# Optimization experiments

Hardware: AMD Instinct MI355X
Metric: run time of the kernel (lower is better)

Reference implementation:

```python
import jax, jax.numpy as jnp
import numpy as np
import math

B, L, HID = 2, 2048, 1024
H, DK, RATIO, SHARED, TOPK = 4, 64, 4, 1, 2
EXP_V = 2
DV = DK * EXP_V
KEY_DIM = H * DK
VAL_DIM = KEY_DIM * EXP_V
HE = H * RATIO
KS = 4
EPS = 1e-5


def _silu(x):
    return x * jax.nn.sigmoid(x)


def _dwconv_causal(x, w):
    # x: (B, L, C), w: (C, KS); causal depthwise short conv
    xp = jnp.pad(x, ((0, 0), (KS - 1, 0), (0, 0))).transpose(0, 2, 1)
    y = jax.lax.conv_general_dilated(xp, w[:, None, :], (1,), 'VALID',
                                     feature_group_count=w.shape[0],
                                     dimension_numbers=('NCH', 'OIH', 'NCH'))
    return y.transpose(0, 2, 1)


def _l2norm(x):
    return x * jax.lax.rsqrt(jnp.sum(x * x, -1, keepdims=True) + 1e-6)


def _forward(hidden_states, Wq, Wk, Wv, Wb, Wa, Wg, Wo, conv_q, conv_k, conv_v,
             Wq_exp, Wk_exp, W_gate, A_log, dt_bias, norm_w):
    x = hidden_states
    q = _silu(_dwconv_causal(x @ Wq.T, conv_q)).reshape(B, L, H, DK)
    k = _silu(_dwconv_causal(x @ Wk.T, conv_k)).reshape(B, L, H, DK)
    v = _silu(_dwconv_causal(x @ Wv.T, conv_v)).reshape(B, L, H, DV)
    # per-head expert expansion -> (B,L,H,RATIO,DK)
    qe = jnp.einsum('blhd,hkd->blhk', q, Wq_exp).reshape(B, L, H, RATIO, DK)
    ke = jnp.einsum('blhd,hkd->blhk', k, Wk_exp).reshape(B, L, H, RATIO, DK)
    qe = _l2norm(qe) * (DK ** -0.5)
    ke = _l2norm(ke)
    # token-policy top-k routing over non-shared experts
    logits = jnp.einsum('blhd,nd->blhn', q, W_gate)
    scores = jax.nn.softmax(logits.astype(jnp.float32), axis=-1)
    tw, ti = jax.lax.top_k(scores, TOPK)
    tw = tw / jnp.sum(tw, -1, keepdims=True)
    full = jnp.sum(jax.nn.one_hot(ti + SHARED, RATIO, dtype=tw.dtype) * tw[..., None], axis=-2)
    full = full.at[..., :SHARED].set(1.0 / SHARED)
    w_r = (full / jnp.sum(full, -1, keepdims=True)).astype(x.dtype)  # (B,L,H,RATIO)
    mask = (w_r > 0).astype(x.dtype)
    beta = jax.nn.sigmoid(x @ Wb.T).reshape(B, L, H, RATIO) * mask
    g = -jnp.exp(A_log).reshape(H, RATIO) * jax.nn.softplus((x @ Wa.T) + dt_bias).reshape(B, L, H, RATIO)
    g = g * mask  # unrouted memories: exp(0)=1, no decay, no update
    # gated delta-rule recurrence over HE = H*RATIO memories
    qs = qe.reshape(B, L, HE, DK).transpose(1, 0, 2, 3)
    ks_ = ke.reshape(B, L, HE, DK).transpose(1, 0, 2, 3)
    vs = jnp.broadcast_to(v[:, :, :, None, :], (B, L, H, RATIO, DV)).reshape(B, L, HE, DV).transpose(1, 0, 2, 3)
    bs = beta.reshape(B, L, HE).transpose(1, 0, 2)
    gs = g.reshape(B, L, HE).transpose(1, 0, 2)

    def step(S, xs):
        qt, kt, vt, bt, gt = xs
        S = S * jnp.exp(gt)[..., None, None]
        kv = jnp.einsum('bhk,bhkv->bhv', kt, S)
        S = S + jnp.einsum('bhk,bhv->bhkv', kt, (vt - kv) * bt[..., None])
        return S, jnp.einsum('bhk,bhkv->bhv', qt, S)

    S0 = jnp.zeros((B, HE, DK, DV), x.dtype)
    _, o = jax.lax.scan(step, S0, (qs, ks_, vs, bs, gs))
    o = o.transpose(1, 0, 2, 3).reshape(B, L, H, RATIO, DV)
    o = jnp.einsum('blhe,blhev->blhv', w_r, o)
    # FusedRMSNormSwishGate + output projection
    gate = (x @ Wg.T).reshape(B, L, H, DV)
    o = o * jax.lax.rsqrt(jnp.mean(o * o, -1, keepdims=True) + EPS) * norm_w * _silu(gate)
    return o.reshape(B, L, VAL_DIM) @ Wo.T


def setup_inputs():
    keys = jax.random.split(jax.random.key(0), 18)
    n = lambda i, shp, sc=1.0: jax.random.normal(keys[i], shp, jnp.float32) * sc
    A = jax.random.uniform(keys[14], (HE,), jnp.float32, 1e-3, 16.0)
    dt = jnp.exp(jax.random.uniform(keys[15], (HE,), jnp.float32) * (math.log(0.1) - math.log(0.001)) + math.log(0.001))
    dt = jnp.clip(dt, 1e-4, None)
    return {
        'hidden_states': n(0, (B, L, HID)),
        'Wq': n(1, (KEY_DIM, HID), HID ** -0.5),
        'Wk': n(2, (KEY_DIM, HID), HID ** -0.5),
        'Wv': n(3, (VAL_DIM, HID), HID ** -0.5),
        'Wb': n(4, (HE, HID), HID ** -0.5),
        'Wa': n(5, (HE, HID), HID ** -0.5),
        'Wg': n(6, (VAL_DIM, HID), HID ** -0.5),
        'Wo': n(7, (HID, VAL_DIM), VAL_DIM ** -0.5),
        'conv_q': n(8, (KEY_DIM, KS), 0.5),
        'conv_k': n(9, (KEY_DIM, KS), 0.5),
        'conv_v': n(10, (VAL_DIM, KS), 0.5),
        'Wq_exp': n(11, (H, RATIO * DK, DK), DK ** -0.5),
        'Wk_exp': n(12, (H, RATIO * DK, DK), DK ** -0.5),
        'W_gate': n(13, (RATIO - SHARED, DK), DK ** -0.5),
        'A_log': jnp.log(A),
        'dt_bias': dt + jnp.log(-jnp.expm1(-dt)),
        'norm_w': jnp.ones((DV,), jnp.float32),
    }


def reference(hidden_states, Wq, Wk, Wv, Wb, Wa, Wg, Wo, conv_q, conv_k, conv_v,
              Wq_exp, Wk_exp, W_gate, A_log, dt_bias, norm_w):
    return _forward(hidden_states, Wq, Wk, Wv, Wb, Wa, Wg, Wo, conv_q, conv_k, conv_v,
                    Wq_exp, Wk_exp, W_gate, A_log, dt_bias, norm_w)
```

## Files before the change

kernel.cpp:

```cpp
#include <hip/hip_runtime.h>
#include <hip/hip_bf16.h>
#include <math.h>

#define B_    2
#define L_    2048
#define HID_  1024
#define H_    4
#define DK_   64
#define RATIO_ 4
#define HE_   16
#define DV_   128
#define T_    64
#define NC_   32
#define SPITCH 72
#define APITCH 68
#define NCAT  1408

typedef __attribute__((ext_vector_type(8))) short short8;
typedef __attribute__((ext_vector_type(4))) float f32x4;

__device__ __forceinline__ float sigmoidf_(float x){ return 1.f/(1.f+expf(-x)); }
__device__ __forceinline__ ushort f2bf(float x){
  __hip_bfloat16 h = __float2bfloat16(x);
  return *reinterpret_cast<ushort*>(&h);
}
__device__ __forceinline__ float bf2f(ushort u){
  union { uint32_t i; float f; } v; v.i = ((uint32_t)u) << 16; return v.f;
}
__device__ __forceinline__ uint32_t pk2(float a, float b){
  return ((uint32_t)f2bf(b) << 16) | f2bf(a);
}
__device__ __forceinline__ void unpk8(uint4 w, float* f){
  f[0]=bf2f((ushort)(w.x&0xffff)); f[1]=bf2f((ushort)(w.x>>16));
  f[2]=bf2f((ushort)(w.y&0xffff)); f[3]=bf2f((ushort)(w.y>>16));
  f[4]=bf2f((ushort)(w.z&0xffff)); f[5]=bf2f((ushort)(w.z>>16));
  f[6]=bf2f((ushort)(w.w&0xffff)); f[7]=bf2f((ushort)(w.w>>16));
}

__global__ __launch_bounds__(256) void cast_bf16(const float* __restrict__ in,
                                                 ushort* __restrict__ out, int n)
{
  int i = blockIdx.x*256 + threadIdx.x;
  if (i < n) out[i] = f2bf(in[i]);
}

__global__ __launch_bounds__(256) void concat_wcat(const float* __restrict__ Wk,
    const float* __restrict__ Wv, const float* __restrict__ Wg,
    const float* __restrict__ Wb, const float* __restrict__ Wa,
    ushort* __restrict__ Wcat)
{
  int idx = blockIdx.x*256 + threadIdx.x;
  if (idx >= NCAT*1024) return;
  int r = idx >> 10, cc = idx & 1023;
  float v = 0.f;
  if      (r < 256)  v = Wk[(size_t)r*1024 + cc];
  else if (r < 768)  v = Wv[(size_t)(r-256)*1024 + cc];
  else if (r < 1280) v = Wg[(size_t)(r-768)*1024 + cc];
  else if (r < 1296) v = Wb[(size_t)(r-1280)*1024 + cc];
  else if (r < 1312) v = Wa[(size_t)(r-1296)*1024 + cc];
  Wcat[idx] = f2bf(v);
}

__global__ __launch_bounds__(256) void gemm_bf16(
    const ushort* __restrict__ A, int lda,
    const ushort* __restrict__ Bm, int ldb,
    float* __restrict__ C, int ldc, int K)
{
  __shared__ ushort As[128*32];
  __shared__ ushort Bs[128*32];
  const int tid  = threadIdx.x;
  const int wave = tid >> 6, lane = tid & 63;
  const int row0 = blockIdx.y*128, col0 = blockIdx.x*128;
  const int wr = (wave >> 1) * 64, wc = (wave & 1) * 64;
  const int frow = lane & 15;
  const int fko  = (lane >> 4) << 3;
  f32x4 acc[4][4];
  #pragma unroll
  for (int i=0;i<4;i++)
    #pragma unroll
    for (int j=0;j<4;j++) acc[i][j] = (f32x4){0.f,0.f,0.f,0.f};
  for (int k0 = 0; k0 < K; k0 += 32) {
    #pragma unroll
    for (int cc = 0; cc < 2; cc++) {
      int c  = wave*128 + cc*64 + lane;
      int r  = c >> 2;
      int ko = (c & 3) << 3;
      __builtin_amdgcn_global_load_lds(
        (const __attribute__((address_space(1))) void*)(A + (size_t)(row0+r)*lda + k0 + ko),
        (__attribute__((address_space(3))) void*)(As + (size_t)(wave*128 + cc*64)*8),
        16, 0, 0);
      __builtin_amdgcn_global_load_lds(
        (const __attribute__((address_space(1))) void*)(Bm + (size_t)(col0+r)*ldb + k0 + ko),
        (__attribute__((address_space(3))) void*)(Bs + (size_t)(wave*128 + cc*64)*8),
        16, 0, 0);
    }
    __syncthreads();
    short8 af[4], bfv[4];
    #pragma unroll
    for (int mi=0;mi<4;mi++)
      af[mi] = *reinterpret_cast<const short8*>(&As[(wr + mi*16 + frow)*32 + fko]);
    #pragma unroll
    for (int ni=0;ni<4;ni++)
      bfv[ni] = *reinterpret_cast<const short8*>(&Bs[(wc + ni*16 + frow)*32 + fko]);
    #pragma unroll
    for (int mi=0;mi<4;mi++)
      #pragma unroll
      for (int ni=0;ni<4;ni++)
        acc[mi][ni] = __builtin_amdgcn_mfma_f32_16x16x32_bf16(af[mi], bfv[ni], acc[mi][ni], 0, 0, 0);
    __syncthreads();
  }
  const int ocol = lane & 15;
  const int orow = (lane >> 4) << 2;
  #pragma unroll
  for (int mi=0;mi<4;mi++)
    #pragma unroll
    for (int ni=0;ni<4;ni++) {
      size_t base = (size_t)(row0 + wr + mi*16 + orow)*ldc + (col0 + wc + ni*16 + ocol);
      #pragma unroll
      for (int q=0;q<4;q++) C[base + (size_t)q*ldc] = acc[mi][ni][q];
    }
}

__global__ __launch_bounds__(256) void gemm_expand_bf16(
    const ushort* __restrict__ qc_bf, const ushort* __restrict__ kc_bf,
    const ushort* __restrict__ Wqeb, const ushort* __restrict__ Wkeb,
    ushort* __restrict__ qeb, ushort* __restrict__ keb)
{
  const int z = blockIdx.z;
  const int hh = z & 3;
  const ushort* A  = (z < 4 ? qc_bf : kc_bf) + hh*64;
  const ushort* Bm = (z < 4 ? Wqeb  : Wkeb ) + (size_t)hh*16384;
  ushort* C        = (z < 4 ? qeb   : keb  ) + hh*256;
  const int lda = 256, ldb = 64, ldc = 1024, K = 64;
  __shared__ ushort As[128*32];
  __shared__ ushort Bs[128*32];
  const int tid  = threadIdx.x;
  const int wave = tid >> 6, lane = tid & 63;
  const int row0 = blockIdx.y*128, col0 = blockIdx.x*128;
  const int wr = (wave >> 1) * 64, wc = (wave & 1) * 64;
  const int frow = lane & 15;
  const int fko  = (lane >> 4) << 3;
  f32x4 acc[4][4];
  #pragma unroll
  for (int i=0;i<4;i++)
    #pragma unroll
    for (int j=0;j<4;j++) acc[i][j] = (f32x4){0.f,0.f,0.f,0.f};
  for (int k0 = 0; k0 < K; k0 += 32) {
    #pragma unroll
    for (int cc = 0; cc < 2; cc++) {
      int c  = wave*128 + cc*64 + lane;
      int r  = c >> 2;
      int ko = (c & 3) << 3;
      __builtin_amdgcn_global_load_lds(
        (const __attribute__((address_space(1))) void*)(A + (size_t)(row0+r)*lda + k0 + ko),
        (__attribute__((address_space(3))) void*)(As + (size_t)(wave*128 + cc*64)*8),
        16, 0, 0);
      __builtin_amdgcn_global_load_lds(
        (const __attribute__((address_space(1))) void*)(Bm + (size_t)(col0+r)*ldb + k0 + ko),
        (__attribute__((address_space(3))) void*)(Bs + (size_t)(wave*128 + cc*64)*8),
        16, 0, 0);
    }
    __syncthreads();
    short8 af[4], bfv[4];
    #pragma unroll
    for (int mi=0;mi<4;mi++)
      af[mi] = *reinterpret_cast<const short8*>(&As[(wr + mi*16 + frow)*32 + fko]);
    #pragma unroll
    for (int ni=0;ni<4;ni++)
      bfv[ni] = *reinterpret_cast<const short8*>(&Bs[(wc + ni*16 + frow)*32 + fko]);
    #pragma unroll
    for (int mi=0;mi<4;mi++)
      #pragma unroll
      for (int ni=0;ni<4;ni++)
        acc[mi][ni] = __builtin_amdgcn_mfma_f32_16x16x32_bf16(af[mi], bfv[ni], acc[mi][ni], 0, 0, 0);
    __syncthreads();
  }
  const int ocol = lane & 15;
  const int orow = (lane >> 4) << 2;
  #pragma unroll
  for (int mi=0;mi<4;mi++)
    #pragma unroll
    for (int ni=0;ni<4;ni++) {
      size_t base = (size_t)(row0 + wr + mi*16 + orow)*ldc + (col0 + wc + ni*16 + ocol);
      #pragma unroll
      for (int q=0;q<4;q++) C[base + (size_t)q*ldc] = f2bf(acc[mi][ni][q]);
    }
}

__global__ __launch_bounds__(256) void gemm_f32_db(const float* __restrict__ A, int lda,
    const float* __restrict__ Bm, int ldb, float* __restrict__ C, int ldc,
    int M, int N, int K)
{
  __shared__ float As[2][32][64];
  __shared__ float Bs[2][32][64];
  const int tid = threadIdx.x;
  const int row0 = blockIdx.y * 64;
  const int col0 = blockIdx.x * 64;
  const int tx = tid & 15, ty = tid >> 4;
  const int r0s = tid >> 3;
  const int k4s = (tid & 7) << 2;
  float4 av0, av1, bv0, bv1;

  av0 = *(const float4*)&A[(size_t)(row0 + r0s)*lda + k4s];
  av1 = *(const float4*)&A[(size_t)(row0 + r0s + 32)*lda + k4s];
  bv0 = (col0 + r0s < N) ? *(const float4*)&Bm[(size_t)(col0 + r0s)*ldb + k4s] : make_float4(0,0,0,0);
  bv1 = (col0 + r0s + 32 < N) ? *(const float4*)&Bm[(size_t)(col0 + r0s + 32)*ldb + k4s] : make_float4(0,0,0,0);
  As[0][k4s+0][r0s] = av0.x; As[0][k4s+1][r0s] = av0.y; As[0][k4s+2][r0s] = av0.z; As[0][k4s+3][r0s] = av0.w;
  As[0][k4s+0][r0s+32] = av1.x; As[0][k4s+1][r0s+32] = av1.y; As[0][k4s+2][r0s+32] = av1.z; As[0][k4s+3][r0s+32] = av1.w;
  Bs[0][k4s+0][r0s] = bv0.x; Bs[0][k4s+1][r0s] = bv0.y; Bs[0][k4s+2][r0s] = bv0.z; Bs[0][k4s+3][r0s] = bv0.w;
  Bs[0][k4s+0][r0s+32] = bv1.x; Bs[0][k4s+1][r0s+32] = bv1.y; Bs[0][k4s+2][r0s+32] = bv1.z; Bs[0][k4s+3][r0s+32] = bv1.w;
  __syncthreads();

  float acc[4][4] = {};
  const int nt = K >> 5;
  for (int kt = 0; kt < nt; ++kt) {
    const int p = kt & 1;
    if (kt + 1 < nt) {
      int k0 = (kt+1) << 5;
      av0 = *(const float4*)&A[(size_t)(row0 + r0s)*lda + k0 + k4s];
      av1 = *(const float4*)&A[(size_t)(row0 + r0s + 32)*lda + k0 + k4s];
      bv0 = (col0 + r0s < N) ? *(const float4*)&Bm[(size_t)(col0 + r0s)*ldb + k0 + k4s] : make_float4(0,0,0,0);
      bv1 = (col0 + r0s + 32 < N) ? *(const float4*)&Bm[(size_t)(col0 + r0s + 32)*ldb + k0 + k4s] : make_float4(0,0,0,0);
    }
    #pragma unroll
    for (int kk = 0; kk < 32; kk++) {
      float4 a4 = *(const float4*)&As[p][kk][ty*4];
      float4 b4 = *(const float4*)&Bs[p][kk][tx*4];
      float a[4] = {a4.x,a4.y,a4.z,a4.w};
      float b[4] = {b4.x,b4.y,b4.z,b4.w};
      #pragma unroll
      for (int i=0;i<4;i++)
        #pragma unroll
        for (int j=0;j<4;j++) acc[i][j] += a[i]*b[j];
    }
    if (kt + 1 < nt) {
      const int q = p ^ 1;
      As[q][k4s+0][r0s] = av0.x; As[q][k4s+1][r0s] = av0.y; As[q][k4s+2][r0s] = av0.z; As[q][k4s+3][r0s] = av0.w;
      As[q][k4s+0][r0s+32] = av1.x; As[q][k4s+1][r0s+32] = av1.y; As[q][k4s+2][r0s+32] = av1.z; As[q][k4s+3][r0s+32] = av1.w;
      Bs[q][k4s+0][r0s] = bv0.x; Bs[q][k4s+1][r0s] = bv0.y; Bs[q][k4s+2][r0s] = bv0.z; Bs[q][k4s+3][r0s] = bv0.w;
      Bs[q][k4s+0][r0s+32] = bv1.x; Bs[q][k4s+1][r0s+32] = bv1.y; Bs[q][k4s+2][r0s+32] = bv1.z; Bs[q][k4s+3][r0s+32] = bv1.w;
    }
    __syncthreads();
  }
  #pragma unroll
  for (int i=0;i<4;i++) {
    int r = row0 + ty*4 + i;
    #pragma unroll
    for (int j=0;j<4;j++) {
      int cc = col0 + tx*4 + j;
      if (cc < N) C[(size_t)r*ldc + cc] = acc[i][j];
    }
  }
}

__global__ __launch_bounds__(256) void conv_silu(const float* __restrict__ in, int ild,
    const float* __restrict__ w, float* __restrict__ outf, ushort* __restrict__ outb,
    int C, int total)
{
  int n = blockIdx.x*256 + threadIdx.x;
  if (n >= total) return;
  int c = n % C;
  int t = (n / C) % L_;
  int b = n / (C*L_);
  float acc = 0.f;
  #pragma unroll
  for (int s = 0; s < 4; s++) {
    int tt = t - 3 + s;
    if (tt >= 0) acc += in[((size_t)b*L_ + tt)*ild + c] * w[c*4+s];
  }
  float y = acc * sigmoidf_(acc);
  if (outf) outf[n] = y;
  if (outb) outb[n] = f2bf(y);
}

__global__ __launch_bounds__(256) void routing(const float* __restrict__ qc,
    const float* __restrict__ kvgba, const float* __restrict__ Wg3,
    const float* __restrict__ A_log, const float* __restrict__ dt_bias,
    float* __restrict__ w_buf, float* __restrict__ bt_T, float* __restrict__ g_T)
{
  int n = blockIdx.x*256 + threadIdx.x;
  int h  = n & 3;
  int bl = n >> 2;
  const float* q = qc + (size_t)bl*256 + h*64;
  float l0=0.f, l1=0.f, l2=0.f;
  for (int d=0; d<64; d++) {
    float qd = q[d];
    l0 += qd*Wg3[d]; l1 += qd*Wg3[64+d]; l2 += qd*Wg3[128+d];
  }
  float mx = fmaxf(l0, fmaxf(l1, l2));
  float e0 = expf(l0-mx), e1 = expf(l1-mx), e2 = expf(l2-mx);
  float inv_s = 1.f/(e0+e1+e2);
  float p0 = e0*inv_s, p1 = e1*inv_s, p2 = e2*inv_s;
  int m1 = 0; float pm1 = p0;
  if (p1 > pm1) { m1 = 1; pm1 = p1; }
  if (p2 > pm1) { m1 = 2; pm1 = p2; }
  int ia = (m1==0) ? 1 : 0;
  int ib = (m1==2) ? 1 : 2;
  float pa = (m1==0) ? p1 : p0;
  float pb = (m1==2) ? p1 : p2;
  int   m2  = (pb > pa) ? ib : ia;
  float pm2 = (pb > pa) ? pb : pa;
  float inv_w = 1.f/(pm1 + pm2);
  float w1 = 0.5f*pm1*inv_w;
  float w2 = 0.5f*pm2*inv_w;
  #pragma unroll
  for (int r = 0; r < 4; r++) {
    float wr = (r==0) ? 0.5f : (((r-1)==m1) ? w1 : (((r-1)==m2) ? w2 : 0.f));
    int he = h*4 + r;
    w_buf[(size_t)bl*16 + he] = wr;
    float mask = (wr > 0.f) ? 1.f : 0.f;
    bt_T[(size_t)he*4096 + bl] = mask * sigmoidf_(kvgba[(size_t)bl*NCAT + 1280 + he]);
    float av = kvgba[(size_t)bl*NCAT + 1296 + he] + dt_bias[he];
    float sp = fmaxf(av, 0.f) + log1pf(expf(-fabsf(av)));
    g_T[(size_t)he*4096 + bl] = -expf(A_log[he]) * sp * mask;
  }
}

__device__ __forceinline__ f32x4 tile64(const ushort* Am, int r0,
                                        const ushort* Bm, int c0, int lane)
{
  f32x4 acc = {0.f,0.f,0.f,0.f};
  const int fr = lane & 15, fo = (lane >> 4) << 3;
  #pragma unroll
  for (int kk = 0; kk < 2; ++kk) {
    short8 a = *reinterpret_cast<const short8*>(&Am[(r0+fr)*SPITCH + fo + kk*32]);
    short8 b = *reinterpret_cast<const short8*>(&Bm[(c0+fr)*SPITCH + fo + kk*32]);
    acc = __builtin_amdgcn_mfma_f32_16x16x32_bf16(a, b, acc, 0, 0, 0);
  }
  return acc;
}

__global__ __launch_bounds__(256,2) void scan_chunk_mfma(
    const ushort* __restrict__ keb, const ushort* __restrict__ qeb,
    const ushort* __restrict__ vcb, const float* __restrict__ bt_T,
    const float* __restrict__ g_T, ushort* __restrict__ o0b,
    ushort* __restrict__ Qtb, ushort* __restrict__ Mcb, ushort* __restrict__ Bcb)
{
  __shared__ float smem[18496];
  ushort* Kbf = (ushort*)smem;
  ushort* Qbf = (ushort*)(smem + 2304);
  ushort* KTD = (ushort*)(smem + 4608);
  float*  Af  = smem + 6912;
  ushort* Pf  = (ushort*)(smem + 6912);
  ushort* UV  = (ushort*)(smem + 11264);
  float*  cgs = smem + 18176;
  float*  bts = cgs + 64;
  float*  bGs = bts + 64;
  float*  Ds  = bGs + 64;
  float*  gams= Ds + 64;

  const int id = blockIdx.x;
  const int c  = id >> 5;
  const int s  = id & 31;
  const int h  = s & 3;
  const int b  = (s >> 2) & 1;
  const int r  = s >> 3;
  const int he = h*4 + r;
  const int bhe = b*HE_ + he;
  const int tid = threadIdx.x;
  const int wave = tid >> 6, lane = tid & 63;
  const size_t l0 = (size_t)b*L_ + (size_t)c*T_;

  const int tr = tid >> 2;
  const int sg = tid & 3;
  float kf[16], qf[16];
  uint4 vw0, vw1, vw2, vw3;
  float sk, sq;
  {
    const uint4* kp = (const uint4*)(keb + (l0+tr)*1024 + he*64 + sg*16);
    const uint4* qp = (const uint4*)(qeb + (l0+tr)*1024 + he*64 + sg*16);
    uint4 kv[2] = {kp[0], kp[1]};
    uint4 qv[2] = {qp[0], qp[1]};
    unpk8(kv[0], kf); unpk8(kv[1], kf+8);
    unpk8(qv[0], qf); unpk8(qv[1], qf+8);
    float ssk = 0.f, ssq = 0.f;
    #pragma unroll
    for (int i=0;i<16;i++){ ssk += kf[i]*kf[i]; ssq += qf[i]*qf[i]; }
    ssk += __shfl_xor(ssk, 1); ssk += __shfl_xor(ssk, 2);
    ssq += __shfl_xor(ssq, 1); ssq += __shfl_xor(ssq, 2);
    sk = rsqrtf(ssk + 1e-6f);
    sq = rsqrtf(ssq + 1e-6f) * 0.125f;
    const uint4* vp = (const uint4*)(vcb + (l0+tr)*512 + h*128 + sg*32);
    vw0 = vp[0]; vw1 = vp[1]; vw2 = vp[2]; vw3 = vp[3];
  }
  if (tid < 64) {
    float g  = g_T[(size_t)he*4096 + l0 + tid];
    float bt = bt_T[(size_t)he*4096 + l0 + tid];
    float cg = g;
    #pragma unroll
    for (int off = 1; off < 64; off <<= 1) {
      float o = __shfl_up(cg, off);
      if (tid >= off) cg += o;
    }
    float cg63 = __shfl(cg, 63);
    cgs[tid] = cg; bts[tid] = bt;
    float gm = expf(cg);
    gams[tid] = gm; bGs[tid] = bt*gm; Ds[tid] = expf(cg63 - cg);
  }
  __syncthreads();
  {
    float Dt = Ds[tr];
    uint2* kdst = (uint2*)(Kbf + tr*SPITCH + sg*16);
    uint2* qdst = (uint2*)(Qbf + tr*SPITCH + sg*16);
    #pragma unroll
    for (int i=0;i<4;i++){
      kdst[i] = make_uint2(pk2(kf[4*i+0]*sk, kf[4*i+1]*sk), pk2(kf[4*i+2]*sk, kf[4*i+3]*sk));
      qdst[i] = make_uint2(pk2(qf[4*i+0]*sq, qf[4*i+1]*sq), pk2(qf[4*i+2]*sq, qf[4*i+3]*sq));
    }
    float skD = sk*Dt;
    #pragma unroll
    for (int i=0;i<16;i++){
      int d = sg*16 + i;
      KTD[d*SPITCH + tr] = f2bf(kf[i]*skD);
    }
    uint4* vdst = (uint4*)(UV + tr*128 + sg*32);
    vdst[0] = vw0; vdst[1] = vw1; vdst[2] = vw2; vdst[3] = vw3;
  }
  __syncthreads();
  {
    const int r0 = wave*16;
    #pragma unroll
    for (int ct=0; ct<4; ++ct) {
      f32x4 acc = tile64(Kbf, r0, Kbf, ct*16, lane);
      int t = r0 + ((lane>>4)<<2);
      int ss = ct*16 + (lane&15);
      #pragma unroll
      for (int q=0;q<4;q++){
        int tq = t + q;
        Af[tq*APITCH + ss] = (ss < tq) ? bts[tq]*expf(cgs[tq]-cgs[ss])*acc[q] : 0.f;
      }
    }
  }
  __syncthreads();
  float u[64];
  if (tid < 192) {
    if (tid < 128) {
      const ushort* Vb = UV;
      #pragma unroll
      for (int ss=0;ss<64;++ss) u[ss] = bts[ss]*bf2f(Vb[ss*128 + tid]);
    } else {
      #pragma unroll
      for (int ss=0;ss<64;++ss) u[ss] = bGs[ss]*bf2f(Kbf[ss*SPITCH + (tid-128)]);
    }
  }
  __syncthreads();
  if (tid < 192) {
    #pragma unroll
    for (int t=1;t<64;++t) {
      const float4* Ar = (const float4*)(Af + t*APITCH);
      float p0=0.f,p1=0.f,p2=0.f,p3=0.f;
      #pragma unroll
      for (int s4=0; s4*4<t; ++s4) {
        float4 a = Ar[s4];
        p0 += a.x*u[s4*4+0]; p1 += a.y*u[s4*4+1];
        p2 += a.z*u[s4*4+2]; p3 += a.w*u[s4*4+3];
      }
      u[t] -= (p0+p1)+(p2+p3);
    }
    ushort* Ut = UV;
    uint4* dst = (uint4*)&Ut[tid*SPITCH];
    #pragma unroll
    for (int i=0;i<8;++i)
      dst[i] = make_uint4(pk2(u[8*i+0],u[8*i+1]), pk2(u[8*i+2],u[8*i+3]),
                          pk2(u[8*i+4],u[8*i+5]), pk2(u[8*i+6],u[8*i+7]));
  }
  __syncthreads();
  {
    const int r0 = wave*16;
    f32x4 accs[4];
    #pragma unroll
    for (int ct=0; ct<4; ++ct) accs[ct] = tile64(Qbf, r0, Kbf, ct*16, lane);
    __syncthreads();
    #pragma unroll
    for (int ct=0; ct<4; ++ct) {
      int t = r0 + ((lane>>4)<<2);
      int ss = ct*16 + (lane&15);
      #pragma unroll
      for (int q=0;q<4;q++){
        int tq = t + q;
        float val = (ss <= tq) ? expf(cgs[tq]-cgs[ss])*accs[ct][q] : 0.f;
        Pf[tq*SPITCH + ss] = f2bf(val);
      }
    }
  }
  __syncthreads();
  {
    const int r0 = wave*16;
    const float gend = expf(cgs[63]);
    const ushort* Ut = UV;
    const ushort* UtK = UV + 128*SPITCH;
    const size_t bb = ((size_t)bhe*NC_ + c)*(size_t)(64*128);
    const size_t pb = ((size_t)bhe*NC_ + c)*(size_t)(64*64);
    #pragma unroll
    for (int jt=0; jt<8; ++jt) {
      f32x4 acc = tile64(Pf, r0, Ut, jt*16, lane);
      int t = r0 + ((lane>>4)<<2);
      int j = jt*16 + (lane&15);
      #pragma unroll
      for (int q=0;q<4;q++)
        o0b[((l0 + t + q)*HE_ + he)*DV_ + j] = f2bf(acc[q]);
    }
    #pragma unroll
    for (int jt=0; jt<8; ++jt) {
      f32x4 acc = tile64(KTD, r0, Ut, jt*16, lane);
      int i = r0 + ((lane>>4)<<2);
      int j = jt*16 + (lane&15);
      #pragma unroll
      for (int q=0;q<4;q++)
        Bcb[bb + (size_t)(i+q)*128 + j] = f2bf(acc[q]);
    }
    #pragma unroll
    for (int ct=0; ct<4; ++ct) {
      f32x4 acc = tile64(KTD, r0, UtK, ct*16, lane);
      int i = r0 + ((lane>>4)<<2);
      int m = ct*16 + (lane&15);
      #pragma unroll
      for (int q=0;q<4;q++){
        float val = -acc[q];
        int row = i + q;
        if (row == m) val += gend;
        int pc = (((m>>3)^(row&7))<<3) | (m&7);
        Mcb[pb + (size_t)row*64 + pc] = f2bf(val);
      }
    }
    #pragma unroll
    for (int ct=0; ct<4; ++ct) {
      f32x4 acc = tile64(Pf, r0, UtK, ct*16, lane);
      int t = r0 + ((lane>>4)<<2);
      int m = ct*16 + (lane&15);
      #pragma unroll
      for (int q=0;q<4;q++){
        int row = t + q;
        int pc = (((m>>3)^(row&7))<<3) | (m&7);
        Qtb[pb + (size_t)row*64 + pc] = f2bf(gams[row]*bf2f(Qbf[row*SPITCH + m]) - acc[q]);
      }
    }
  }
}

__device__ __forceinline__ void stage_qm(const ushort* __restrict__ src, ushort* dst,
                                         int wave, int lane)
{
  #pragma unroll
  for (int pass = 0; pass < 2; ++pass){
    int idx = pass*256 + wave*64 + lane;
    __builtin_amdgcn_global_load_lds(
      (const __attribute__((address_space(1))) void*)(src + (size_t)idx*8),
      (__attribute__((address_space(3))) void*)(dst + (size_t)idx*8), 16, 0, 0);
  }
}

__global__ __launch_bounds__(256) void compose_correct(
    const ushort* __restrict__ Mcb, const ushort* __restrict__ Bcb,
    const ushort* __restrict__ Qtb, ushort* __restrict__ o_corrb)
{
  __shared__ ushort Ql[2][4096];
  __shared__ ushort Ml[2][4096];
  __shared__ float SSl[1024];
  const int s   = blockIdx.x;
  const int h   = s & 3;
  const int b   = (s >> 2) & 1;
  const int r   = s >> 3;
  const int he  = h*4 + r;
  const int bhe = b*HE_ + he;
  const int j0  = blockIdx.y * 16;
  const int tid = threadIdx.x;
  const int wave = tid >> 6, lane = tid & 63;
  const int rw = tid >> 2;
  const int jg = tid & 3;
  const int rsw = rw & 7;

  for (int id = tid; id < 1024; id += 256) SSl[id] = 0.f;

  stage_qm(Mcb + (size_t)(bhe*NC_)*4096, Ml[0], wave, lane);
  float4 bcur;
  {
    uint2 bw = *(const uint2*)&Bcb[(size_t)(bhe*NC_)*8192 + rw*128 + j0 + jg*4];
    bcur = make_float4(bf2f((ushort)(bw.x&0xffff)), bf2f((ushort)(bw.x>>16)),
                       bf2f((ushort)(bw.y&0xffff)), bf2f((ushort)(bw.y>>16)));
  }
  __syncthreads();

  int p = 0;
  for (int c = 0; c < NC_; ++c){
    float4 bnext = make_float4(0.f,0.f,0.f,0.f);
    if (c+1 < NC_){
      stage_qm(Qtb + (size_t)(bhe*NC_ + c + 1)*4096, Ql[p^1], wave, lane);
      if (c+1 < NC_-1){
        stage_qm(Mcb + (size_t)(bhe*NC_ + c + 1)*4096, Ml[p^1], wave, lane);
        uint2 bw = *(const uint2*)&Bcb[(size_t)(bhe*NC_ + c + 1)*8192 + rw*128 + j0 + jg*4];
        bnext = make_float4(bf2f((ushort)(bw.x&0xffff)), bf2f((ushort)(bw.x>>16)),
                            bf2f((ushort)(bw.y&0xffff)), bf2f((ushort)(bw.y>>16)));
      }
    }
    const float4* SS4 = (const float4*)SSl;
    float4 oa = make_float4(0.f,0.f,0.f,0.f);
    if (c > 0){
      const ushort* Qr = Ql[p] + rw*64;
      #pragma unroll
      for (int gb = 0; gb < 8; ++gb){
        uint4 w = *(const uint4*)&Qr[(gb ^ rsw) << 3];
        float f[8]; unpk8(w, f);
        #pragma unroll
        for (int e = 0; e < 8; ++e){
          float4 sv = SS4[(gb*8+e)*4 + jg];
          oa.x += f[e]*sv.x; oa.y += f[e]*sv.y; oa.z += f[e]*sv.z; oa.w += f[e]*sv.w;
        }
      }
    }
    {
      size_t oi = (((size_t)b*L_ + c*T_ + rw)*HE_ + he)*DV_ + j0 + jg*4;
      *(uint2*)&o_corrb[oi] = make_uint2(pk2(oa.x, oa.y), pk2(oa.z, oa.w));
    }
    float4 ns = bcur;
    if (c < NC_-1){
      const ushort* Mr = Ml[p] + rw*64;
      #pragma unroll
      for (int gb = 0; gb < 8; ++gb){
        uint4 w = *(const uint4*)&Mr[(gb ^ rsw) << 3];
        float f[8]; unpk8(w, f);
        #pragma unroll
        for (int e = 0; e < 8; ++e){
          float4 sv = SS4[(gb*8+e)*4 + jg];
          ns.x += f[e]*sv.x; ns.y += f[e]*sv.y; ns.z += f[e]*sv.z; ns.w += f[e]*sv.w;
        }
      }
    }
    __syncthreads();
    if (c < NC_-1) *(float4*)&SSl[rw*16 + jg*4] = ns;
    __syncthreads();
    p ^= 1;
    bcur = bnext;
  }
}

__global__ __launch_bounds__(128) void combine(const ushort* __restrict__ o0b,
    const ushort* __restrict__ o_corrb, const float* __restrict__ w_buf,
    const float* __restrict__ kvgba, const float* __restrict__ norm_w,
    ushort* __restrict__ o_fin)
{
  int n  = blockIdx.x;
  int h  = n & 3;
  int bl = n >> 2;
  int j  = threadIdx.x;
  size_t wb = (size_t)bl*16 + h*4;
  size_t ob = wb*128 + j;
  float oc = 0.f;
  #pragma unroll
  for (int r = 0; r < 4; r++){
    size_t oi = ob + (size_t)r*128;
    oc += w_buf[wb+r] * (bf2f(o0b[oi]) + bf2f(o_corrb[oi]));
  }
  float ss = oc*oc;
  #pragma unroll
  for (int off = 32; off > 0; off >>= 1) ss += __shfl_xor(ss, off);
  __shared__ float red[2];
  if ((threadIdx.x & 63) == 0) red[threadIdx.x >> 6] = ss;
  __syncthreads();
  float mean = (red[0] + red[1]) * (1.f/128.f);
  float sc = rsqrtf(mean + 1e-5f);
  float gv = kvgba[(size_t)bl*NCAT + 768 + h*128 + j];
  o_fin[(size_t)bl*512 + h*128 + j] = f2bf(oc * sc * norm_w[j] * (gv * sigmoidf_(gv)));
}

extern "C" void kernel_launch(void* const* d_in, const int* in_sizes, int n_in,
                              void* d_out, int out_size, void* d_ws, size_t ws_size,
                              hipStream_t stream)
{
  (void)in_sizes; (void)n_in; (void)out_size; (void)ws_size;
  const float* x       = (const float*)d_in[0];
  const float* Wq      = (const float*)d_in[1];
  const float* Wk      = (const float*)d_in[2];
  const float* Wv      = (const float*)d_in[3];
  const float* Wb      = (const float*)d_in[4];
  const float* Wa      = (const float*)d_in[5];
  const float* Wg      = (const float*)d_in[6];
  const float* Wo      = (const float*)d_in[7];
  const float* conv_q  = (const float*)d_in[8];
  const float* conv_k  = (const float*)d_in[9];
  const float* conv_v  = (const float*)d_in[10];
  const float* Wq_exp  = (const float*)d_in[11];
  const float* Wk_exp  = (const float*)d_in[12];
  const float* W_gate  = (const float*)d_in[13];
  const float* A_log   = (const float*)d_in[14];
  const float* dt_bias = (const float*)d_in[15];
  const float* norm_w  = (const float*)d_in[16];
  float* out = (float*)d_out;

  const size_t BL = (size_t)B_*L_;
  float* p = (float*)d_ws;
  float* q_lin  = p; p += BL*256;
  float* kvgba  = p; p += BL*NCAT;
  float* q_conv = p; p += BL*256;
  float* w_buf  = p; p += BL*16;
  float* bt_T   = p; p += BL*16;
  float* g_T    = p; p += BL*16;
  ushort* o0b   = (ushort*)p; p += BL*16*64;
  ushort* o_corrb=(ushort*)p; p += BL*16*64;
  ushort* Mcb   = (ushort*)p; p += (size_t)B_*HE_*NC_*2048;
  ushort* Qtb   = (ushort*)p; p += (size_t)B_*HE_*NC_*2048;
  ushort* Bcb   = (ushort*)p; p += (size_t)B_*HE_*NC_*4096;
  ushort* v_convb=(ushort*)p; p += BL*256;
  ushort* xb    = (ushort*)p; p += BL*512;
  ushort* Wcat  = (ushort*)p; p += (NCAT*1024)/2;
  ushort* qc_bf = (ushort*)p; p += BL*128;
  ushort* kc_bf = (ushort*)p; p += BL*128;
  ushort* qeb   = (ushort*)p; p += BL*512;
  ushort* keb   = (ushort*)p; p += BL*512;
  ushort* Wqeb  = (ushort*)p; p += 32768;
  ushort* Wkeb  = (ushort*)p; p += 32768;
  ushort* Wob   = (ushort*)p; p += 262144;
  ushort* o_finb= (ushort*)p; p += BL*256;

  concat_wcat<<<dim3((NCAT*1024+255)/256), dim3(256), 0, stream>>>(Wk, Wv, Wg, Wb, Wa, Wcat);
  { int n = (int)(BL*1024); cast_bf16<<<dim3((n+255)/256), dim3(256), 0, stream>>>(x, xb, n); }
  { int n = 65536;  cast_bf16<<<dim3((n+255)/256), dim3(256), 0, stream>>>(Wq_exp, Wqeb, n); }
  { int n = 65536;  cast_bf16<<<dim3((n+255)/256), dim3(256), 0, stream>>>(Wk_exp, Wkeb, n); }
  { int n = 524288; cast_bf16<<<dim3((n+255)/256), dim3(256), 0, stream>>>(Wo, Wob, n); }

  gemm_f32_db<<<dim3(4, 64), dim3(256), 0, stream>>>(x, 1024, Wq, 1024, q_lin, 256, 4096, 256, 1024);
  gemm_bf16<<<dim3(NCAT/128, 32), dim3(256), 0, stream>>>(xb, 1024, Wcat, 1024, kvgba, NCAT, 1024);

  { int tot = B_*L_*256; conv_silu<<<dim3((tot+255)/256), dim3(256), 0, stream>>>(q_lin, 256, conv_q, q_conv, qc_bf, 256, tot); }
  { int tot = B_*L_*256; conv_silu<<<dim3((tot+255)/256), dim3(256), 0, stream>>>(kvgba, NCAT, conv_k, (float*)nullptr, kc_bf, 256, tot); }
  { int tot = B_*L_*512; conv_silu<<<dim3((tot+255)/256), dim3(256), 0, stream>>>(kvgba + 256, NCAT, conv_v, (float*)nullptr, v_convb, 512, tot); }

  routing<<<dim3(64), dim3(256), 0, stream>>>(q_conv, kvgba, W_gate, A_log, dt_bias,
                                              w_buf, bt_T, g_T);

  gemm_expand_bf16<<<dim3(2, 32, 8), dim3(256), 0, stream>>>(qc_bf, kc_bf, Wqeb, Wkeb, qeb, keb);

  scan_chunk_mfma<<<dim3(NC_*HE_*B_), dim3(256), 0, stream>>>(keb, qeb, v_convb, bt_T, g_T,
                                                              o0b, Qtb, Mcb, Bcb);
  compose_correct<<<dim3(32, 8), dim3(256), 0, stream>>>(Mcb, Bcb, Qtb, o_corrb);
  combine<<<dim3(B_*L_*H_), dim3(128), 0, stream>>>(o0b, o_corrb, w_buf, kvgba, norm_w, o_finb);

  gemm_bf16<<<dim3(8, 32), dim3(256), 0, stream>>>(o_finb, 512, Wob, 512, out, 1024, 512);
}
```

Measured before the change: 358.1 us.

## Stage scan outputs in LDS for coalesced stores; split compose into single-wave blocks

In the chunk scan kernel, the o0 and Bc tiles are now written into shared memory first and then copied out to global memory as 16-byte vectorised stores, replacing scattered 2-byte stores. The compose_correct kernel is restructured from 256-thread blocks covering 16 value columns to 64-thread single-wave blocks covering 8 columns, which doubles the grid. Each thread now owns a full row and 8 columns. The aim is better store coalescing and more parallel blocks for the serial chunk recurrence, at the cost of extra syncs and reuse of shared memory in the scan kernel, and more redundant M/Q staging per block in compose.

```diff
diff --git a/kernel.cpp b/kernel.cpp
--- a/kernel.cpp
+++ b/kernel.cpp
@@ -486,33 +486,16 @@
   __syncthreads();
   {
     const int r0 = wave*16;
+    const int orow = (lane >> 4) << 2;
     const float gend = expf(cgs[63]);
     const ushort* Ut = UV;
     const ushort* UtK = UV + 128*SPITCH;
     const size_t bb = ((size_t)bhe*NC_ + c)*(size_t)(64*128);
     const size_t pb = ((size_t)bhe*NC_ + c)*(size_t)(64*64);
     #pragma unroll
-    for (int jt=0; jt<8; ++jt) {
-      f32x4 acc = tile64(Pf, r0, Ut, jt*16, lane);
-      int t = r0 + ((lane>>4)<<2);
-      int j = jt*16 + (lane&15);
-      #pragma unroll
-      for (int q=0;q<4;q++)
-        o0b[((l0 + t + q)*HE_ + he)*DV_ + j] = f2bf(acc[q]);
-    }
-    #pragma unroll
-    for (int jt=0; jt<8; ++jt) {
-      f32x4 acc = tile64(KTD, r0, Ut, jt*16, lane);
-      int i = r0 + ((lane>>4)<<2);
-      int j = jt*16 + (lane&15);
-      #pragma unroll
-      for (int q=0;q<4;q++)
-        Bcb[bb + (size_t)(i+q)*128 + j] = f2bf(acc[q]);
-    }
-    #pragma unroll
     for (int ct=0; ct<4; ++ct) {
       f32x4 acc = tile64(KTD, r0, UtK, ct*16, lane);
-      int i = r0 + ((lane>>4)<<2);
+      int i = r0 + orow;
       int m = ct*16 + (lane&15);
       #pragma unroll
       for (int q=0;q<4;q++){
@@ -526,7 +509,7 @@
     #pragma unroll
     for (int ct=0; ct<4; ++ct) {
       f32x4 acc = tile64(Pf, r0, UtK, ct*16, lane);
-      int t = r0 + ((lane>>4)<<2);
+      int t = r0 + orow;
       int m = ct*16 + (lane&15);
       #pragma unroll
       for (int q=0;q<4;q++){
@@ -535,66 +518,94 @@
         Qtb[pb + (size_t)row*64 + pc] = f2bf(gams[row]*bf2f(Qbf[row*SPITCH + m]) - acc[q]);
       }
     }
-  }
-}
-
-__device__ __forceinline__ void stage_qm(const ushort* __restrict__ src, ushort* dst,
-                                         int wave, int lane)
-{
-  #pragma unroll
-  for (int pass = 0; pass < 2; ++pass){
-    int idx = pass*256 + wave*64 + lane;
+    __syncthreads();
+    ushort* O0s = (ushort*)smem;
+    #pragma unroll
+    for (int jt=0; jt<8; ++jt) {
+      f32x4 acc = tile64(Pf, r0, Ut, jt*16, lane);
+      int t = r0 + orow;
+      int j = jt*16 + (lane&15);
+      #pragma unroll
+      for (int q=0;q<4;q++) O0s[(t+q)*128 + j] = f2bf(acc[q]);
+    }
+    __syncthreads();
+    ushort* BCs = (ushort*)Af;
+    #pragma unroll
+    for (int jt=0; jt<8; ++jt) {
+      f32x4 acc = tile64(KTD, r0, Ut, jt*16, lane);
+      int i = r0 + orow;
+      int j = jt*16 + (lane&15);
+      #pragma unroll
+      for (int q=0;q<4;q++) BCs[(i+q)*128 + j] = f2bf(acc[q]);
+    }
+    __syncthreads();
+    #pragma unroll
+    for (int idx = tid; idx < 1024; idx += 256) {
+      int row = idx >> 4, seg = idx & 15;
+      *(uint4*)&o0b[((l0 + row)*HE_ + he)*DV_ + seg*8] = *(const uint4*)&O0s[row*128 + seg*8];
+      *(uint4*)&Bcb[bb + (size_t)row*128 + seg*8]      = *(const uint4*)&BCs[row*128 + seg*8];
+    }
+  }
+}
+
+__device__ __forceinline__ void stage_qm64(const ushort* __restrict__ src, ushort* dst,
+                                           int lane)
+{
+  #pragma unroll
+  for (int pass = 0; pass < 8; ++pass){
+    int idx = pass*64 + lane;
     __builtin_amdgcn_global_load_lds(
       (const __attribute__((address_space(1))) void*)(src + (size_t)idx*8),
       (__attribute__((address_space(3))) void*)(dst + (size_t)idx*8), 16, 0, 0);
   }
 }
 
-__global__ __launch_bounds__(256) void compose_correct(
+__global__ __launch_bounds__(64) void compose_correct(
     const ushort* __restrict__ Mcb, const ushort* __restrict__ Bcb,
     const ushort* __restrict__ Qtb, ushort* __restrict__ o_corrb)
 {
   __shared__ ushort Ql[2][4096];
   __shared__ ushort Ml[2][4096];
-  __shared__ float SSl[1024];
+  __shared__ float SSl[512];
   const int s   = blockIdx.x;
   const int h   = s & 3;
   const int b   = (s >> 2) & 1;
   const int r   = s >> 3;
   const int he  = h*4 + r;
   const int bhe = b*HE_ + he;
-  const int j0  = blockIdx.y * 16;
+  const int j0  = blockIdx.y * 8;
   const int tid = threadIdx.x;
-  const int wave = tid >> 6, lane = tid & 63;
-  const int rw = tid >> 2;
-  const int jg = tid & 3;
+  const int rw  = tid;
   const int rsw = rw & 7;
 
-  for (int id = tid; id < 1024; id += 256) SSl[id] = 0.f;
-
-  stage_qm(Mcb + (size_t)(bhe*NC_)*4096, Ml[0], wave, lane);
-  float4 bcur;
+  #pragma unroll
+  for (int idx = tid; idx < 512; idx += 64) SSl[idx] = 0.f;
+
+  stage_qm64(Mcb + (size_t)(bhe*NC_)*4096, Ml[0], tid);
+  float4 bcur0, bcur1;
   {
-    uint2 bw = *(const uint2*)&Bcb[(size_t)(bhe*NC_)*8192 + rw*128 + j0 + jg*4];
-    bcur = make_float4(bf2f((ushort)(bw.x&0xffff)), bf2f((ushort)(bw.x>>16)),
-                       bf2f((ushort)(bw.y&0xffff)), bf2f((ushort)(bw.y>>16)));
+    uint4 bw = *(const uint4*)&Bcb[(size_t)(bhe*NC_)*8192 + rw*128 + j0];
+    float f[8]; unpk8(bw, f);
+    bcur0 = make_float4(f[0],f[1],f[2],f[3]);
+    bcur1 = make_float4(f[4],f[5],f[6],f[7]);
   }
   __syncthreads();
 
   int p = 0;
   for (int c = 0; c < NC_; ++c){
-    float4 bnext = make_float4(0.f,0.f,0.f,0.f);
+    float4 bnext0 = make_float4(0,0,0,0), bnext1 = make_float4(0,0,0,0);
     if (c+1 < NC_){
-      stage_qm(Qtb + (size_t)(bhe*NC_ + c + 1)*4096, Ql[p^1], wave, lane);
+      stage_qm64(Qtb + (size_t)(bhe*NC_ + c + 1)*4096, Ql[p^1], tid);
       if (c+1 < NC_-1){
-        stage_qm(Mcb + (size_t)(bhe*NC_ + c + 1)*4096, Ml[p^1], wave, lane);
-        uint2 bw = *(const uint2*)&Bcb[(size_t)(bhe*NC_ + c + 1)*8192 + rw*128 + j0 + jg*4];
-        bnext = make_float4(bf2f((ushort)(bw.x&0xffff)), bf2f((ushort)(bw.x>>16)),
-                            bf2f((ushort)(bw.y&0xffff)), bf2f((ushort)(bw.y>>16)));
+        stage_qm64(Mcb + (size_t)(bhe*NC_ + c + 1)*4096, Ml[p^1], tid);
+        uint4 bw = *(const uint4*)&Bcb[(size_t)(bhe*NC_ + c + 1)*8192 + rw*128 + j0];
+        float f[8]; unpk8(bw, f);
+        bnext0 = make_float4(f[0],f[1],f[2],f[3]);
+        bnext1 = make_float4(f[4],f[5],f[6],f[7]);
       }
     }
     const float4* SS4 = (const float4*)SSl;
-    float4 oa = make_float4(0.f,0.f,0.f,0.f);
+    float4 oa0 = make_float4(0,0,0,0), oa1 = make_float4(0,0,0,0);
     if (c > 0){
       const ushort* Qr = Ql[p] + rw*64;
       #pragma unroll
@@ -603,16 +614,19 @@
         float f[8]; unpk8(w, f);
         #pragma unroll
         for (int e = 0; e < 8; ++e){
-          float4 sv = SS4[(gb*8+e)*4 + jg];
-          oa.x += f[e]*sv.x; oa.y += f[e]*sv.y; oa.z += f[e]*sv.z; oa.w += f[e]*sv.w;
+          float4 s0 = SS4[(gb*8+e)*2 + 0];
+          float4 s1 = SS4[(gb*8+e)*2 + 1];
+          oa0.x += f[e]*s0.x; oa0.y += f[e]*s0.y; oa0.z += f[e]*s0.z; oa0.w += f[e]*s0.w;
+          oa1.x += f[e]*s1.x; oa1.y += f[e]*s1.y; oa1.z += f[e]*s1.z; oa1.w += f[e]*s1.w;
         }
       }
     }
     {
-      size_t oi = (((size_t)b*L_ + c*T_ + rw)*HE_ + he)*DV_ + j0 + jg*4;
-      *(uint2*)&o_corrb[oi] = make_uint2(pk2(oa.x, oa.y), pk2(oa.z, oa.w));
-    }
-    float4 ns = bcur;
+      size_t oi = (((size_t)b*L_ + c*T_ + rw)*HE_ + he)*DV_ + j0;
+      *(uint4*)&o_corrb[oi] = make_uint4(pk2(oa0.x,oa0.y), pk2(oa0.z,oa0.w),
+                                         pk2(oa1.x,oa1.y), pk2(oa1.z,oa1.w));
+    }
+    float4 ns0 = bcur0, ns1 = bcur1;
     if (c < NC_-1){
       const ushort* Mr = Ml[p] + rw*64;
       #pragma unroll
@@ -621,16 +635,21 @@
         float f[8]; unpk8(w, f);
         #pragma unroll
         for (int e = 0; e < 8; ++e){
-          float4 sv = SS4[(gb*8+e)*4 + jg];
-          ns.x += f[e]*sv.x; ns.y += f[e]*sv.y; ns.z += f[e]*sv.z; ns.w += f[e]*sv.w;
+          float4 s0 = SS4[(gb*8+e)*2 + 0];
+          float4 s1 = SS4[(gb*8+e)*2 + 1];
+          ns0.x += f[e]*s0.x; ns0.y += f[e]*s0.y; ns0.z += f[e]*s0.z; ns0.w += f[e]*s0.w;
+          ns1.x += f[e]*s1.x; ns1.y += f[e]*s1.y; ns1.z += f[e]*s1.z; ns1.w += f[e]*s1.w;
         }
       }
     }
     __syncthreads();
-    if (c < NC_-1) *(float4*)&SSl[rw*16 + jg*4] = ns;
+    if (c < NC_-1){
+      *(float4*)&SSl[rw*8]     = ns0;
+      *(float4*)&SSl[rw*8 + 4] = ns1;
+    }
     __syncthreads();
     p ^= 1;
-    bcur = bnext;
+    bcur0 = bnext0; bcur1 = bnext1;
   }
 }
 
@@ -732,7 +751,7 @@
 
   scan_chunk_mfma<<<dim3(NC_*HE_*B_), dim3(256), 0, stream>>>(keb, qeb, v_convb, bt_T, g_T,
                                                               o0b, Qtb, Mcb, Bcb);
-  compose_correct<<<dim3(32, 8), dim3(256), 0, stream>>>(Mcb, Bcb, Qtb, o_corrb);
+  compose_correct<<<dim3(32, 16), dim3(64), 0, stream>>>(Mcb, Bcb, Qtb, o_corrb);
   combine<<<dim3(B_*L_*H_), dim3(128), 0, stream>>>(o0b, o_corrb, w_buf, kvgba, norm_w, o_finb);
 
   gemm_bf16<<<dim3(8, 32), dim3(256), 0, stream>>>(o_finb, 512, Wob, 512, out, 1024, 512);
```

After: 418.2 us. 1.17x slower.
